# Performance work log

Hardware: AMD Instinct MI355X
Metric: run time of the kernel (lower is better)

## Reference

```python
import jax, jax.numpy as jnp
import numpy as np

NUM_HEADS = 16
HEAD_DIM = 128
CHUNK = 256
ROPE_BASE = 10000.0


def rotate_half(x):
    x1 = x[..., ::2]
    x2 = x[..., 1::2]
    return jnp.stack((-x2, x1), axis=-1).reshape(x.shape)


def rope_cos_sin(seq_len, head_dim):
    inv_freq = 1.0 / (ROPE_BASE ** (np.arange(0, head_dim, 2, dtype=np.float32) / head_dim))
    pos = np.arange(seq_len, dtype=np.float32)
    freqs = np.outer(pos, inv_freq)                  # [S, D/2]
    emb = np.concatenate([freqs, freqs], axis=-1)    # [S, D]
    return jnp.asarray(np.cos(emb)), jnp.asarray(np.sin(emb))


def setup_inputs() -> dict:
    key = jax.random.key(0)
    k1, k2, k3 = jax.random.split(key, 3)
    B, S, E = 2, 4096, 2048
    x = jax.random.normal(k1, (B, S, E), dtype=jnp.float32)
    W_qkv = jax.random.normal(k2, (3 * E, E), dtype=jnp.float32) * 0.02
    W_out = jax.random.normal(k3, (E, E), dtype=jnp.float32) * 0.02
    return {"x": x, "W_qkv": W_qkv, "W_out": W_out}


def reference(x, W_qkv, W_out):
    B, S, E = x.shape
    H, D = NUM_HEADS, HEAD_DIM
    qkv = x @ W_qkv.T                                  # [B,S,3E]
    qkv = qkv.reshape(B, S, 3, H, D).transpose(2, 0, 3, 1, 4)  # [3,B,H,S,D]
    q, k, v = qkv[0], qkv[1], qkv[2]

    cos, sin = rope_cos_sin(S, D)                      # [S,D]
    cos = cos[None, None]
    sin = sin[None, None]
    q = q * cos + rotate_half(q) * sin
    k = k * cos + rotate_half(k) * sin

    # ELU+1 feature map
    q = jax.nn.elu(q) + 1.0
    k = jax.nn.elu(k) + 1.0

    n_chunks = S // CHUNK
    # [n,B,H,C,D]
    to_chunks = lambda t: t.reshape(B, H, n_chunks, CHUNK, D).transpose(2, 0, 1, 3, 4)
    qs, ks, vs = to_chunks(q), to_chunks(k), to_chunks(v)

    tril = jnp.tril(jnp.ones((CHUNK, CHUNK), dtype=x.dtype))  # inclusive causal mask

    def step(carry, qkv_c):
        S_c, Z_c = carry
        qc, kc, vc = qkv_c
        att = jnp.einsum('bhld,bhmd->bhlm', qc, kc) * tril       # intra-chunk causal scores
        num = jnp.einsum('bhlm,bhme->bhle', att, vc) + jnp.einsum('bhld,bhde->bhle', qc, S_c)
        den = att.sum(-1) + jnp.einsum('bhld,bhd->bhl', qc, Z_c)
        S_new = S_c + jnp.einsum('bhld,bhle->bhde', kc, vc)
        Z_new = Z_c + kc.sum(axis=2)
        return (S_new, Z_new), (num, den)

    S0 = jnp.zeros((B, H, D, D), dtype=x.dtype)
    Z0 = jnp.zeros((B, H, D), dtype=x.dtype)
    _, (num, den) = jax.lax.scan(step, (S0, Z0), (qs, ks, vs))
    # num: [n,B,H,C,D] -> [B,H,S,D]; den: [n,B,H,C] -> [B,H,S]
    num = num.transpose(1, 2, 0, 3, 4).reshape(B, H, S, D)
    den = den.transpose(1, 2, 0, 3).reshape(B, H, S)
    den = jnp.maximum(den, 1e-6)

    out = num / den[..., None]                          # [B,H,S,D]
    out = out.transpose(0, 2, 1, 3).reshape(B, S, H * D)
    return out @ W_out.T
```

## Files before the change

kernel.cpp:

```cpp
#include <hip/hip_runtime.h>
#include <cmath>

#define Ss 4096
#define NCh 16
#define CK 256

typedef unsigned short bfu;
typedef __bf16 bf16x8 __attribute__((ext_vector_type(8)));
typedef float f32x4 __attribute__((ext_vector_type(4)));
typedef unsigned short u16x8 __attribute__((ext_vector_type(8)));

__device__ __forceinline__ float bf2f(unsigned short u) {
    union { unsigned u32; float f; } v; v.u32 = ((unsigned)u) << 16; return v.f;
}
__device__ __forceinline__ unsigned short f2bf(float f) {
    union { float f; unsigned u; } v; v.f = f;
    unsigned r = v.u + 0x7fff + ((v.u >> 16) & 1);
    return (unsigned short)(r >> 16);
}

__device__ __forceinline__ void g2l16(void* lds, const void* g) {
    __builtin_amdgcn_global_load_lds(
        (const __attribute__((address_space(1))) void*)g,
        (__attribute__((address_space(3))) void*)lds, 16, 0, 0);
}

#define MFMA __builtin_amdgcn_mfma_f32_16x16x32_bf16

__global__ void rope_table(float* __restrict__ cosT, float* __restrict__ sinT) {
    int id = blockIdx.x * 256 + threadIdx.x;
    int f = id & 63, s = id >> 6;
    float e = (2.0f * (float)f) / 128.0f;
    float inv = 1.0f / powf(10000.0f, e);
    float ang = (float)s * inv;
    cosT[id] = cosf(ang);
    sinT[id] = sinf(ang);
}

__global__ void conv2_bf16(const float* __restrict__ a, bfu* __restrict__ oa, int n4a,
                           const float* __restrict__ b, bfu* __restrict__ ob, int n4b) {
    const int total = n4a + n4b;
    for (int i = blockIdx.x * 256 + threadIdx.x; i < total; i += gridDim.x * 256) {
        const float* in; bfu* out; int j;
        if (i < n4a) { in = a; out = oa; j = i; }
        else         { in = b; out = ob; j = i - n4a; }
        float4 v = ((const float4*)in)[j];
        ushort4 o;
        o.x = f2bf(v.x); o.y = f2bf(v.y); o.z = f2bf(v.z); o.w = f2bf(v.w);
        ((ushort4*)out)[j] = o;
    }
}
__global__ void conv_bf16(const float* __restrict__ in, bfu* __restrict__ out, int n4) {
    for (int i = blockIdx.x * 256 + threadIdx.x; i < n4; i += gridDim.x * 256) {
        float4 v = ((const float4*)in)[i];
        ushort4 o;
        o.x = f2bf(v.x); o.y = f2bf(v.y); o.z = f2bf(v.z); o.w = f2bf(v.w);
        ((ushort4*)out)[i] = o;
    }
}

template<int EPI>
__global__ __launch_bounds__(512) void gemm256(
    const bfu* __restrict__ A, const bfu* __restrict__ B, int nbx,
    const float* __restrict__ cosT, const float* __restrict__ sinT,
    bfu* __restrict__ qb, bfu* __restrict__ kb,
    bfu* __restrict__ kT, bfu* __restrict__ vT,
    float* __restrict__ outF)
{
    __shared__ bfu AsL[2 * 256 * 64];
    __shared__ bfu BsL[2 * 256 * 64];
    const int nwg = gridDim.x;
    const int q8 = nwg >> 3;
    const int swz = (blockIdx.x & 7) * q8 + (blockIdx.x >> 3);
    const int bm = (swz / nbx) * 256, bn = (swz % nbx) * 256;

    const int tid = threadIdx.x;
    const int wid = tid >> 6, lane = tid & 63;
    const int wm = wid >> 2, wn = wid & 3;
    const int l15 = lane & 15, l7 = lane & 7, lhi = lane >> 4;

    const int rl = tid >> 3;
    const int scol = ((tid & 7) ^ (rl & 7)) * 8;
    const bfu* Ab = A + (size_t)(bm + rl) * 2048 + scol;
    const bfu* Bb = B + (size_t)(bn + rl) * 2048 + scol;

    f32x4 acc[8][4] = {};

    auto stageA = [&](int T) {
        bfu* d = AsL + (T & 1) * 16384 + wid * 512;
        const bfu* s = Ab + (size_t)T * 64;
        g2l16(d,         s);
        g2l16(d + 4096,  s + (size_t)64 * 2048);
        g2l16(d + 8192,  s + (size_t)128 * 2048);
        g2l16(d + 12288, s + (size_t)192 * 2048);
    };
    auto stageB = [&](int T) {
        bfu* d = BsL + (T & 1) * 16384 + wid * 512;
        const bfu* s = Bb + (size_t)T * 64;
        g2l16(d,         s);
        g2l16(d + 4096,  s + (size_t)64 * 2048);
        g2l16(d + 8192,  s + (size_t)128 * 2048);
        g2l16(d + 12288, s + (size_t)192 * 2048);
    };

    stageA(0); stageB(0);
    stageA(1); stageB(1);
    asm volatile("s_waitcnt vmcnt(8)" ::: "memory");
    __builtin_amdgcn_s_barrier();
    asm volatile("" ::: "memory");

    for (int T = 0; T < 32; ++T) {
        const char* Ax = (const char*)AsL + (T & 1) * 32768;
        const char* Bx = (const char*)BsL + (T & 1) * 32768;
        bf16x8 a0[4][2], a1[4][2], b0[2][2], b1[2][2];

#pragma unroll
        for (int mi = 0; mi < 4; ++mi)
#pragma unroll
            for (int ks = 0; ks < 2; ++ks)
                a0[mi][ks] = *(const bf16x8*)(Ax + (wm * 128 + mi * 16 + l15) * 128 + (((ks * 4 + lhi) ^ l7) << 4));
#pragma unroll
        for (int ni = 0; ni < 2; ++ni)
#pragma unroll
            for (int ks = 0; ks < 2; ++ks)
                b0[ni][ks] = *(const bf16x8*)(Bx + (wn * 64 + ni * 16 + l15) * 128 + (((ks * 4 + lhi) ^ l7) << 4));
        asm volatile("s_waitcnt lgkmcnt(0)" ::: "memory");
        __builtin_amdgcn_sched_barrier(0);
        __builtin_amdgcn_s_setprio(1);
#pragma unroll
        for (int mi = 0; mi < 4; ++mi)
#pragma unroll
            for (int ni = 0; ni < 2; ++ni) {
                acc[mi][ni] = MFMA(a0[mi][0], b0[ni][0], acc[mi][ni], 0, 0, 0);
                acc[mi][ni] = MFMA(a0[mi][1], b0[ni][1], acc[mi][ni], 0, 0, 0);
            }
        __builtin_amdgcn_s_setprio(0);

#pragma unroll
        for (int ni = 0; ni < 2; ++ni)
#pragma unroll
            for (int ks = 0; ks < 2; ++ks)
                b1[ni][ks] = *(const bf16x8*)(Bx + (wn * 64 + (ni + 2) * 16 + l15) * 128 + (((ks * 4 + lhi) ^ l7) << 4));
        asm volatile("s_waitcnt lgkmcnt(0)" ::: "memory");
        __builtin_amdgcn_sched_barrier(0);
        __builtin_amdgcn_s_setprio(1);
#pragma unroll
        for (int mi = 0; mi < 4; ++mi)
#pragma unroll
            for (int ni = 0; ni < 2; ++ni) {
                acc[mi][ni + 2] = MFMA(a0[mi][0], b1[ni][0], acc[mi][ni + 2], 0, 0, 0);
                acc[mi][ni + 2] = MFMA(a0[mi][1], b1[ni][1], acc[mi][ni + 2], 0, 0, 0);
            }
        __builtin_amdgcn_s_setprio(0);
        __builtin_amdgcn_s_barrier();
        asm volatile("" ::: "memory");

#pragma unroll
        for (int mi = 0; mi < 4; ++mi)
#pragma unroll
            for (int ks = 0; ks < 2; ++ks)
                a1[mi][ks] = *(const bf16x8*)(Ax + (wm * 128 + (mi + 4) * 16 + l15) * 128 + (((ks * 4 + lhi) ^ l7) << 4));
        if (T < 30) stageB(T + 2);
        asm volatile("s_waitcnt lgkmcnt(0)" ::: "memory");
        __builtin_amdgcn_sched_barrier(0);
        __builtin_amdgcn_s_setprio(1);
#pragma unroll
        for (int mi = 0; mi < 4; ++mi)
#pragma unroll
            for (int ni = 0; ni < 2; ++ni) {
                acc[mi + 4][ni] = MFMA(a1[mi][0], b0[ni][0], acc[mi + 4][ni], 0, 0, 0);
                acc[mi + 4][ni] = MFMA(a1[mi][1], b0[ni][1], acc[mi + 4][ni], 0, 0, 0);
            }
        __builtin_amdgcn_s_setprio(0);
        __builtin_amdgcn_s_barrier();
        asm volatile("" ::: "memory");

        if (T < 30) stageA(T + 2);
        __builtin_amdgcn_s_setprio(1);
#pragma unroll
        for (int mi = 0; mi < 4; ++mi)
#pragma unroll
            for (int ni = 0; ni < 2; ++ni) {
                acc[mi + 4][ni + 2] = MFMA(a1[mi][0], b1[ni][0], acc[mi + 4][ni + 2], 0, 0, 0);
                acc[mi + 4][ni + 2] = MFMA(a1[mi][1], b1[ni][1], acc[mi + 4][ni + 2], 0, 0, 0);
            }
        __builtin_amdgcn_s_setprio(0);
        if (T < 30) { asm volatile("s_waitcnt vmcnt(8)" ::: "memory"); }
        else        { asm volatile("s_waitcnt vmcnt(0)" ::: "memory"); }
        __builtin_amdgcn_s_barrier();
        asm volatile("" ::: "memory");
    }

    if constexpr (EPI == 0) {
        const int part = bn >> 11;
#pragma unroll
        for (int mi = 0; mi < 8; ++mi) {
            const int m0 = bm + wm * 128 + mi * 16 + (lhi << 2);
            const int bq = m0 >> 12;
            const int sloc = m0 & 4095;
#pragma unroll
            for (int ni = 0; ni < 4; ++ni) {
                const int cp = (bn & 2047) + wn * 64 + ni * 16 + l15;
                const int d = cp & 127;
                const int head = cp >> 7;
                const int f = d & 63;
                float vv[4];
#pragma unroll
                for (int r = 0; r < 4; ++r) {
                    float v = acc[mi][ni][r];
                    float p = __shfl_xor(v, 1);
                    if (part < 2) {
                        const int s = (m0 + r) & 4095;
                        float cc = cosT[s * 64 + f], sn = sinT[s * 64 + f];
                        float o = (d & 1) ? v * cc + p * sn : v * cc - p * sn;
                        v = o > 0.0f ? o + 1.0f : __expf(o);
                    }
                    vv[r] = v;
                }
                if (part == 0) {
#pragma unroll
                    for (int r = 0; r < 4; ++r)
                        qb[(size_t)(m0 + r) * 2048 + cp] = f2bf(vv[r]);
                } else if (part == 1) {
#pragma unroll
                    for (int r = 0; r < 4; ++r)
                        kb[(size_t)(m0 + r) * 2048 + cp] = f2bf(vv[r]);
                    ushort4 t4;
                    t4.x = f2bf(vv[0]); t4.y = f2bf(vv[1]); t4.z = f2bf(vv[2]); t4.w = f2bf(vv[3]);
                    *(ushort4*)(kT + ((size_t)(bq * 16 + head) * 128 + d) * 4096 + sloc) = t4;
                } else {
                    ushort4 t4;
                    t4.x = f2bf(vv[0]); t4.y = f2bf(vv[1]); t4.z = f2bf(vv[2]); t4.w = f2bf(vv[3]);
                    *(ushort4*)(vT + ((size_t)(bq * 16 + head) * 128 + d) * 4096 + sloc) = t4;
                }
            }
        }
    } else {
#pragma unroll
        for (int mi = 0; mi < 8; ++mi) {
            const int m0 = bm + wm * 128 + mi * 16 + (lhi << 2);
#pragma unroll
            for (int ni = 0; ni < 4; ++ni) {
                const int n = bn + wn * 64 + ni * 16 + l15;
#pragma unroll
                for (int r = 0; r < 4; ++r)
                    outF[(size_t)(m0 + r) * 2048 + n] = acc[mi][ni][r];
            }
        }
    }
}

__global__ __launch_bounds__(256) void kv_outer_mfma(
    const bfu* __restrict__ vT, const bfu* __restrict__ kT,
    bfu* __restrict__ Scb, float* __restrict__ Zc)
{
    __shared__ bfu As[128 * 64];
    __shared__ bfu Bs[128 * 64];
    __shared__ float zS[128][2];
    const int batch = blockIdx.x;
    const int c = batch & 15, h = (batch >> 4) & 15, b = batch >> 8;
    const size_t fbase = (size_t)(b * 16 + h) * 128 * 4096 + c * 256;
    const int tid = threadIdx.x, wid = tid >> 6, lane = tid & 63;
    const int wr = wid >> 1, wc = wid & 1;
    const int srow = lane >> 3, scol = (lane & 7) * 8;
    f32x4 acc[4][4] = {};
    float zreg = 0.0f;
    const int zd = tid >> 1, zo = (tid & 1) * 32;

    for (int k0 = 0; k0 < 256; k0 += 64) {
        __syncthreads();
#pragma unroll
        for (int i = 0; i < 4; ++i) {
            const int r = i * 32 + wid * 8;
            g2l16(&As[r * 64], vT + fbase + (size_t)(r + srow) * 4096 + k0 + scol);
            g2l16(&Bs[r * 64], kT + fbase + (size_t)(r + srow) * 4096 + k0 + scol);
        }
        __syncthreads();
#pragma unroll
        for (int ks = 0; ks < 2; ++ks) {
            bf16x8 af[4], bfr[4];
#pragma unroll
            for (int mi = 0; mi < 4; ++mi)
                af[mi] = *(const bf16x8*)&As[(wr * 64 + mi * 16 + (lane & 15)) * 64 + ks * 32 + (lane >> 4) * 8];
#pragma unroll
            for (int ni = 0; ni < 4; ++ni)
                bfr[ni] = *(const bf16x8*)&Bs[(wc * 64 + ni * 16 + (lane & 15)) * 64 + ks * 32 + (lane >> 4) * 8];
#pragma unroll
            for (int mi = 0; mi < 4; ++mi)
#pragma unroll
                for (int ni = 0; ni < 4; ++ni)
                    acc[mi][ni] = MFMA(af[mi], bfr[ni], acc[mi][ni], 0, 0, 0);
        }
#pragma unroll
        for (int j = 0; j < 32; ++j) zreg += bf2f(Bs[zd * 64 + zo + j]);
    }
    zS[zd][tid & 1] = zreg;
    __syncthreads();
    if (tid < 128) Zc[(size_t)batch * 128 + tid] = zS[tid][0] + zS[tid][1];
    bfu* Sout = Scb + (size_t)batch * 16384;
#pragma unroll
    for (int mi = 0; mi < 4; ++mi)
#pragma unroll
        for (int ni = 0; ni < 4; ++ni) {
            const int d = wc * 64 + ni * 16 + (lane & 15);
#pragma unroll
            for (int r = 0; r < 4; ++r) {
                const int e = wr * 64 + mi * 16 + ((lane >> 4) << 2) + r;
                Sout[e * 128 + d] = f2bf(acc[mi][ni][r]);
            }
        }
}

__global__ void prefix_Sb(bfu* __restrict__ Scb) {
    size_t idx = (size_t)blockIdx.x * 256 + threadIdx.x;
    size_t bh = idx >> 14, de = idx & 16383;
    bfu* p = Scb + bh * (size_t)NCh * 16384 + de;
    float run = 0.0f;
#pragma unroll
    for (int c = 0; c < NCh; ++c) {
        float t = bf2f(p[(size_t)c * 16384]);
        p[(size_t)c * 16384] = f2bf(run);
        run += t;
    }
}
__global__ void prefix_Z(float* __restrict__ Zc) {
    size_t idx = (size_t)blockIdx.x * 256 + threadIdx.x;
    size_t bh = idx >> 7, d = idx & 127;
    float* p = Zc + bh * (size_t)NCh * 128 + d;
    float run = 0.0f;
#pragma unroll
    for (int c = 0; c < NCh; ++c) {
        float t = p[(size_t)c * 128];
        p[(size_t)c * 128] = run;
        run += t;
    }
}

__global__ __launch_bounds__(256) void chunk_mfma(
    const bfu* __restrict__ qb, const bfu* __restrict__ kb,
    const bfu* __restrict__ vT, const bfu* __restrict__ Scb,
    const float* __restrict__ Zc, bfu* __restrict__ ao)
{
    __shared__ bfu shrd[16384];
    __shared__ bfu attL[16384];
    __shared__ float Zs[128];
    __shared__ float denS[128][2];
    const int half = blockIdx.x, batch = blockIdx.y;
    const int c = batch & 15, h = (batch >> 4) & 15, b = batch >> 8;
    const int row0 = b * Ss + c * CK;
    const int tid = threadIdx.x, wid = tid >> 6, lane = tid & 63;
    const int wr = wid >> 1, wc = wid & 1;
    const int sr = lane >> 4, sc8 = (lane & 15) * 8;
    if (tid < 128) Zs[tid] = Zc[(size_t)batch * 128 + tid];

    bf16x8 qf[4][4];
    {
        const bfu* qrow = qb + (size_t)(row0 + half * 128 + wr * 64 + (lane & 15)) * 2048
                          + h * 128 + (lane >> 4) * 8;
#pragma unroll
        for (int mi = 0; mi < 4; ++mi)
#pragma unroll
            for (int ks = 0; ks < 4; ++ks)
                qf[mi][ks] = *(const bf16x8*)(qrow + (size_t)mi * 16 * 2048 + ks * 32);
    }
    f32x4 num[4][4] = {};
    float den_reg = 0.0f;
    const int dl = tid >> 1, dc0 = (tid & 1) * 64;

    for (int kb_ = 0; kb_ <= half; ++kb_) {
        __syncthreads();
#pragma unroll
        for (int i = 0; i < 8; ++i) {
            const int r = i * 16 + wid * 4;
            g2l16(&shrd[r * 128], kb + (size_t)(row0 + kb_ * 128 + r + sr) * 2048 + h * 128 + sc8);
        }
        __syncthreads();
        f32x4 attacc[4][4] = {};
#pragma unroll
        for (int ks = 0; ks < 4; ++ks) {
            bf16x8 bfr[4];
#pragma unroll
            for (int ni = 0; ni < 4; ++ni)
                bfr[ni] = *(const bf16x8*)&shrd[(wc * 64 + ni * 16 + (lane & 15)) * 128 + ks * 32 + (lane >> 4) * 8];
#pragma unroll
            for (int mi = 0; mi < 4; ++mi)
#pragma unroll
                for (int ni = 0; ni < 4; ++ni)
                    attacc[mi][ni] = MFMA(qf[mi][ks], bfr[ni], attacc[mi][ni], 0, 0, 0);
        }
        __syncthreads();
#pragma unroll
        for (int i = 0; i < 8; ++i) {
            const int r = i * 16 + wid * 4;
            g2l16(&shrd[r * 128],
                  vT + ((size_t)(b * 16 + h) * 128 + r + sr) * 4096 + c * 256 + kb_ * 128 + sc8);
        }
        const bool needmask = (kb_ == half);
#pragma unroll
        for (int mi = 0; mi < 4; ++mi)
#pragma unroll
            for (int ni = 0; ni < 4; ++ni) {
                const int l0 = wr * 64 + mi * 16 + ((lane >> 4) << 2);
                const int m = wc * 64 + ni * 16 + (lane & 15);
#pragma unroll
                for (int r = 0; r < 4; ++r) {
                    const int l = l0 + r;
                    float v = attacc[mi][ni][r];
                    if (needmask && (half * 128 + l) < (kb_ * 128 + m)) v = 0.0f;
                    const int byte = (l * 256 + m * 2) ^ ((l & 7) << 4);
                    *(bfu*)((char*)attL + byte) = f2bf(v);
                }
            }
        __syncthreads();
#pragma unroll
        for (int ks = 0; ks < 4; ++ks) {
            bf16x8 af[4], bfr[4];
#pragma unroll
            for (int mi = 0; mi < 4; ++mi) {
                const int l = wr * 64 + mi * 16 + (lane & 15);
                const int byte = (l * 256 + (ks * 32 + (lane >> 4) * 8) * 2) ^ ((l & 7) << 4);
                af[mi] = *(const bf16x8*)((const char*)attL + byte);
            }
#pragma unroll
            for (int ni = 0; ni < 4; ++ni)
                bfr[ni] = *(const bf16x8*)&shrd[(wc * 64 + ni * 16 + (lane & 15)) * 128 + ks * 32 + (lane >> 4) * 8];
#pragma unroll
            for (int mi = 0; mi < 4; ++mi)
#pragma unroll
                for (int ni = 0; ni < 4; ++ni)
                    num[mi][ni] = MFMA(af[mi], bfr[ni], num[mi][ni], 0, 0, 0);
        }
#pragma unroll
        for (int j8 = 0; j8 < 8; ++j8) {
            const int byte = (dl * 256 + (dc0 + j8 * 8) * 2) ^ ((dl & 7) << 4);
            u16x8 a = *(const u16x8*)((const char*)attL + byte);
#pragma unroll
            for (int jj = 0; jj < 8; ++jj) den_reg += bf2f(a[jj]);
        }
    }
    __syncthreads();
#pragma unroll
    for (int i = 0; i < 8; ++i) {
        const int r = i * 16 + wid * 4;
        g2l16(&shrd[r * 128], Scb + (size_t)batch * 16384 + (size_t)(r + sr) * 128 + sc8);
    }
    __syncthreads();
#pragma unroll
    for (int ks = 0; ks < 4; ++ks) {
        bf16x8 bfr[4];
#pragma unroll
        for (int ni = 0; ni < 4; ++ni)
            bfr[ni] = *(const bf16x8*)&shrd[(wc * 64 + ni * 16 + (lane & 15)) * 128 + ks * 32 + (lane >> 4) * 8];
#pragma unroll
        for (int mi = 0; mi < 4; ++mi)
#pragma unroll
            for (int ni = 0; ni < 4; ++ni)
                num[mi][ni] = MFMA(qf[mi][ks], bfr[ni], num[mi][ni], 0, 0, 0);
    }
    {
        const bfu* qrow = qb + (size_t)(row0 + half * 128 + dl) * 2048 + h * 128 + dc0;
#pragma unroll
        for (int j8 = 0; j8 < 8; ++j8) {
            u16x8 a = *(const u16x8*)(qrow + j8 * 8);
#pragma unroll
            for (int jj = 0; jj < 8; ++jj) den_reg += bf2f(a[jj]) * Zs[dc0 + j8 * 8 + jj];
        }
    }
    denS[dl][tid & 1] = den_reg;
    __syncthreads();
    bfu* aop = ao + (size_t)(row0 + half * 128) * 2048 + h * 128;
#pragma unroll
    for (int mi = 0; mi < 4; ++mi)
#pragma unroll
        for (int ni = 0; ni < 4; ++ni) {
            const int e = wc * 64 + ni * 16 + (lane & 15);
#pragma unroll
            for (int r = 0; r < 4; ++r) {
                const int l = wr * 64 + mi * 16 + ((lane >> 4) << 2) + r;
                float dv = denS[l][0] + denS[l][1];
                dv = dv > 1e-6f ? dv : 1e-6f;
                aop[(size_t)l * 2048 + e] = f2bf(num[mi][ni][r] / dv);
            }
        }
}

extern "C" void kernel_launch(void* const* d_in, const int* in_sizes, int n_in,
                              void* d_out, int out_size, void* d_ws, size_t ws_size,
                              hipStream_t stream)
{
    const float* x    = (const float*)d_in[0];
    const float* Wqkv = (const float*)d_in[1];
    const float* Wout = (const float*)d_in[2];
    float* out = (float*)d_out;
    char* ws = (char*)d_ws;

    bfu* xb   = (bfu*)(ws);
    bfu* ao   = (bfu*)(ws);
    bfu* wqb  = (bfu*)(ws + 33554432);
    bfu* wob  = (bfu*)(ws + 33554432);
    float* cosT = (float*)(ws + 58720256);
    float* sinT = (float*)(ws + 59768832);
    bfu* Scb  = (bfu*)(ws + 60817408);
    float* Zc = (float*)(ws + 77594624);
    bfu* qb   = (bfu*)(ws + 77856768);
    bfu* kb   = (bfu*)(ws + 111411200);
    bfu* kTb  = (bfu*)(ws + 144965632);
    bfu* vTb  = (bfu*)(ws + 178520064);

    rope_table<<<1024, 256, 0, stream>>>(cosT, sinT);
    conv2_bf16<<<2048, 256, 0, stream>>>(x, xb, 4194304, Wqkv, wqb, 3145728);
    gemm256<0><<<768, 512, 0, stream>>>(xb, wqb, 24, cosT, sinT, qb, kb, kTb, vTb, nullptr);
    conv_bf16<<<1024, 256, 0, stream>>>(Wout, wob, 1048576);
    kv_outer_mfma<<<512, 256, 0, stream>>>(vTb, kTb, Scb, Zc);
    prefix_Z<<<16, 256, 0, stream>>>(Zc);
    prefix_Sb<<<2048, 256, 0, stream>>>(Scb);
    chunk_mfma<<<dim3(2, 512), 256, 0, stream>>>(qb, kb, vTb, Scb, Zc, ao);
    gemm256<1><<<256, 512, 0, stream>>>(ao, wob, 8, nullptr, nullptr, nullptr, nullptr, nullptr, nullptr, out);
}
```

Baseline: 469.6 us.

## Load GEMM A operand directly from global into registers, bypassing LDS

The A tile is no longer staged through LDS. Each wave now loads its 128-row A slice straight from global memory into registers, prefetching one K-step ahead in two halves interleaved with the MFMA blocks. B stays in a double-buffered LDS stage, with prefetch distance cut from two steps to one and fewer barriers per iteration. This removes the A-side LDS writes and reads and halves shared-memory use. In exchange, the four waves that share a row block each fetch the same A rows, multiplying global/L2 traffic, and global load latency is less hidden.

```diff
diff --git a/kernel.cpp b/kernel.cpp
--- a/kernel.cpp
+++ b/kernel.cpp
@@ -67,7 +67,6 @@
     bfu* __restrict__ kT, bfu* __restrict__ vT,
     float* __restrict__ outF)
 {
-    __shared__ bfu AsL[2 * 256 * 64];
     __shared__ bfu BsL[2 * 256 * 64];
     const int nwg = gridDim.x;
     const int q8 = nwg >> 3;
@@ -81,19 +80,14 @@
 
     const int rl = tid >> 3;
     const int scol = ((tid & 7) ^ (rl & 7)) * 8;
-    const bfu* Ab = A + (size_t)(bm + rl) * 2048 + scol;
     const bfu* Bb = B + (size_t)(bn + rl) * 2048 + scol;
 
+    const bfu* Aw = A + (size_t)(bm + wm * 128 + l15) * 2048 + lhi * 8;
+
     f32x4 acc[8][4] = {};
-
-    auto stageA = [&](int T) {
-        bfu* d = AsL + (T & 1) * 16384 + wid * 512;
-        const bfu* s = Ab + (size_t)T * 64;
-        g2l16(d,         s);
-        g2l16(d + 4096,  s + (size_t)64 * 2048);
-        g2l16(d + 8192,  s + (size_t)128 * 2048);
-        g2l16(d + 12288, s + (size_t)192 * 2048);
-    };
+    bf16x8 a[8][2];
+    bf16x8 b0[2][2], b1[2][2];
+
     auto stageB = [&](int T) {
         bfu* d = BsL + (T & 1) * 16384 + wid * 512;
         const bfu* s = Bb + (size_t)T * 64;
@@ -102,23 +96,26 @@
         g2l16(d + 8192,  s + (size_t)128 * 2048);
         g2l16(d + 12288, s + (size_t)192 * 2048);
     };
-
-    stageA(0); stageB(0);
-    stageA(1); stageB(1);
-    asm volatile("s_waitcnt vmcnt(8)" ::: "memory");
+    auto loadA = [&](int T, int h) {
+#pragma unroll
+        for (int mi = 0; mi < 4; ++mi)
+#pragma unroll
+            for (int ks = 0; ks < 2; ++ks)
+                a[h * 4 + mi][ks] = *(const bf16x8*)(Aw + (size_t)(h * 4 + mi) * 16 * 2048
+                                                     + (size_t)T * 64 + ks * 32);
+    };
+
+    stageB(0);
+    __builtin_amdgcn_sched_barrier(0);
+    loadA(0, 0); loadA(0, 1);
+    __builtin_amdgcn_sched_barrier(0);
+    asm volatile("s_waitcnt vmcnt(16)" ::: "memory");
     __builtin_amdgcn_s_barrier();
     asm volatile("" ::: "memory");
 
     for (int T = 0; T < 32; ++T) {
-        const char* Ax = (const char*)AsL + (T & 1) * 32768;
         const char* Bx = (const char*)BsL + (T & 1) * 32768;
-        bf16x8 a0[4][2], a1[4][2], b0[2][2], b1[2][2];
-
-#pragma unroll
-        for (int mi = 0; mi < 4; ++mi)
-#pragma unroll
-            for (int ks = 0; ks < 2; ++ks)
-                a0[mi][ks] = *(const bf16x8*)(Ax + (wm * 128 + mi * 16 + l15) * 128 + (((ks * 4 + lhi) ^ l7) << 4));
+
 #pragma unroll
         for (int ni = 0; ni < 2; ++ni)
 #pragma unroll
@@ -131,8 +128,8 @@
         for (int mi = 0; mi < 4; ++mi)
 #pragma unroll
             for (int ni = 0; ni < 2; ++ni) {
-                acc[mi][ni] = MFMA(a0[mi][0], b0[ni][0], acc[mi][ni], 0, 0, 0);
-                acc[mi][ni] = MFMA(a0[mi][1], b0[ni][1], acc[mi][ni], 0, 0, 0);
+                acc[mi][ni] = MFMA(a[mi][0], b0[ni][0], acc[mi][ni], 0, 0, 0);
+                acc[mi][ni] = MFMA(a[mi][1], b0[ni][1], acc[mi][ni], 0, 0, 0);
             }
         __builtin_amdgcn_s_setprio(0);
 
@@ -148,45 +145,41 @@
         for (int mi = 0; mi < 4; ++mi)
 #pragma unroll
             for (int ni = 0; ni < 2; ++ni) {
-                acc[mi][ni + 2] = MFMA(a0[mi][0], b1[ni][0], acc[mi][ni + 2], 0, 0, 0);
-                acc[mi][ni + 2] = MFMA(a0[mi][1], b1[ni][1], acc[mi][ni + 2], 0, 0, 0);
+                acc[mi][ni + 2] = MFMA(a[mi][0], b1[ni][0], acc[mi][ni + 2], 0, 0, 0);
+                acc[mi][ni + 2] = MFMA(a[mi][1], b1[ni][1], acc[mi][ni + 2], 0, 0, 0);
             }
         __builtin_amdgcn_s_setprio(0);
-        __builtin_amdgcn_s_barrier();
-        asm volatile("" ::: "memory");
-
-#pragma unroll
-        for (int mi = 0; mi < 4; ++mi)
-#pragma unroll
-            for (int ks = 0; ks < 2; ++ks)
-                a1[mi][ks] = *(const bf16x8*)(Ax + (wm * 128 + (mi + 4) * 16 + l15) * 128 + (((ks * 4 + lhi) ^ l7) << 4));
-        if (T < 30) stageB(T + 2);
-        asm volatile("s_waitcnt lgkmcnt(0)" ::: "memory");
-        __builtin_amdgcn_sched_barrier(0);
+
+        if (T < 31) {
+            stageB(T + 1);
+            __builtin_amdgcn_sched_barrier(0);
+            loadA(T + 1, 0);
+            __builtin_amdgcn_sched_barrier(0);
+        }
         __builtin_amdgcn_s_setprio(1);
 #pragma unroll
         for (int mi = 0; mi < 4; ++mi)
 #pragma unroll
             for (int ni = 0; ni < 2; ++ni) {
-                acc[mi + 4][ni] = MFMA(a1[mi][0], b0[ni][0], acc[mi + 4][ni], 0, 0, 0);
-                acc[mi + 4][ni] = MFMA(a1[mi][1], b0[ni][1], acc[mi + 4][ni], 0, 0, 0);
+                acc[mi + 4][ni] = MFMA(a[mi + 4][0], b0[ni][0], acc[mi + 4][ni], 0, 0, 0);
+                acc[mi + 4][ni] = MFMA(a[mi + 4][1], b0[ni][1], acc[mi + 4][ni], 0, 0, 0);
             }
         __builtin_amdgcn_s_setprio(0);
-        __builtin_amdgcn_s_barrier();
-        asm volatile("" ::: "memory");
-
-        if (T < 30) stageA(T + 2);
+
         __builtin_amdgcn_s_setprio(1);
 #pragma unroll
         for (int mi = 0; mi < 4; ++mi)
 #pragma unroll
             for (int ni = 0; ni < 2; ++ni) {
-                acc[mi + 4][ni + 2] = MFMA(a1[mi][0], b1[ni][0], acc[mi + 4][ni + 2], 0, 0, 0);
-                acc[mi + 4][ni + 2] = MFMA(a1[mi][1], b1[ni][1], acc[mi + 4][ni + 2], 0, 0, 0);
+                acc[mi + 4][ni + 2] = MFMA(a[mi + 4][0], b1[ni][0], acc[mi + 4][ni + 2], 0, 0, 0);
+                acc[mi + 4][ni + 2] = MFMA(a[mi + 4][1], b1[ni][1], acc[mi + 4][ni + 2], 0, 0, 0);
             }
         __builtin_amdgcn_s_setprio(0);
-        if (T < 30) { asm volatile("s_waitcnt vmcnt(8)" ::: "memory"); }
-        else        { asm volatile("s_waitcnt vmcnt(0)" ::: "memory"); }
+        if (T < 31) {
+            loadA(T + 1, 1);
+            __builtin_amdgcn_sched_barrier(0);
+            asm volatile("s_waitcnt vmcnt(8)" ::: "memory");
+        }
         __builtin_amdgcn_s_barrier();
         asm volatile("" ::: "memory");
     }
```

New measurement: 723.5 us. 1.54x slower.

## Use 4-wave GEMM with 128x128 per-wave tiles and pipelined A fragment loads

Applied to the files above, without the earlier changes.

The 256x256 GEMM block drops from 8 waves to 4, so each wave computes a 128x128 output tile with 64 accumulators. All B fragments are held in registers and A fragments are double-buffered in groups, with partial lgkmcnt waits to overlap LDS reads with MFMA. Both A and B tiles are now staged once per K step after a barrier, rather than interleaved between MFMA phases. This raises register-level data reuse and cuts LDS read traffic per MFMA. The cost is heavy VGPR/AGPR pressure, one block per CU, and less overlap of global loads with compute.

```diff
diff --git a/kernel.cpp b/kernel.cpp
--- a/kernel.cpp
+++ b/kernel.cpp
@@ -60,7 +60,7 @@
 }
 
 template<int EPI>
-__global__ __launch_bounds__(512) void gemm256(
+__global__ __launch_bounds__(256, 1) void gemm256(
     const bfu* __restrict__ A, const bfu* __restrict__ B, int nbx,
     const float* __restrict__ cosT, const float* __restrict__ sinT,
     bfu* __restrict__ qb, bfu* __restrict__ kb,
@@ -76,7 +76,7 @@
 
     const int tid = threadIdx.x;
     const int wid = tid >> 6, lane = tid & 63;
-    const int wm = wid >> 2, wn = wid & 3;
+    const int wm = wid >> 1, wn = wid & 1;
     const int l15 = lane & 15, l7 = lane & 7, lhi = lane >> 4;
 
     const int rl = tid >> 3;
@@ -84,109 +84,77 @@
     const bfu* Ab = A + (size_t)(bm + rl) * 2048 + scol;
     const bfu* Bb = B + (size_t)(bn + rl) * 2048 + scol;
 
-    f32x4 acc[8][4] = {};
+    f32x4 acc[8][8] = {};
+    bf16x8 bfr[8][2];
+    bf16x8 av[2][2][2];
 
     auto stageA = [&](int T) {
         bfu* d = AsL + (T & 1) * 16384 + wid * 512;
         const bfu* s = Ab + (size_t)T * 64;
-        g2l16(d,         s);
-        g2l16(d + 4096,  s + (size_t)64 * 2048);
-        g2l16(d + 8192,  s + (size_t)128 * 2048);
-        g2l16(d + 12288, s + (size_t)192 * 2048);
+#pragma unroll
+        for (int i = 0; i < 8; ++i)
+            g2l16(d + i * 2048, s + (size_t)i * 32 * 2048);
     };
     auto stageB = [&](int T) {
         bfu* d = BsL + (T & 1) * 16384 + wid * 512;
         const bfu* s = Bb + (size_t)T * 64;
-        g2l16(d,         s);
-        g2l16(d + 4096,  s + (size_t)64 * 2048);
-        g2l16(d + 8192,  s + (size_t)128 * 2048);
-        g2l16(d + 12288, s + (size_t)192 * 2048);
+#pragma unroll
+        for (int i = 0; i < 8; ++i)
+            g2l16(d + i * 2048, s + (size_t)i * 32 * 2048);
     };
 
     stageA(0); stageB(0);
     stageA(1); stageB(1);
-    asm volatile("s_waitcnt vmcnt(8)" ::: "memory");
+    asm volatile("s_waitcnt vmcnt(16)" ::: "memory");
     __builtin_amdgcn_s_barrier();
     asm volatile("" ::: "memory");
 
     for (int T = 0; T < 32; ++T) {
         const char* Ax = (const char*)AsL + (T & 1) * 32768;
         const char* Bx = (const char*)BsL + (T & 1) * 32768;
-        bf16x8 a0[4][2], a1[4][2], b0[2][2], b1[2][2];
-
-#pragma unroll
-        for (int mi = 0; mi < 4; ++mi)
+
+#pragma unroll
+        for (int ni = 0; ni < 8; ++ni)
 #pragma unroll
             for (int ks = 0; ks < 2; ++ks)
-                a0[mi][ks] = *(const bf16x8*)(Ax + (wm * 128 + mi * 16 + l15) * 128 + (((ks * 4 + lhi) ^ l7) << 4));
-#pragma unroll
-        for (int ni = 0; ni < 2; ++ni)
+                bfr[ni][ks] = *(const bf16x8*)(Bx + (wn * 128 + ni * 16 + l15) * 128 + (((ks * 4 + lhi) ^ l7) << 4));
+#pragma unroll
+        for (int mi2 = 0; mi2 < 2; ++mi2)
 #pragma unroll
             for (int ks = 0; ks < 2; ++ks)
-                b0[ni][ks] = *(const bf16x8*)(Bx + (wn * 64 + ni * 16 + l15) * 128 + (((ks * 4 + lhi) ^ l7) << 4));
-        asm volatile("s_waitcnt lgkmcnt(0)" ::: "memory");
-        __builtin_amdgcn_sched_barrier(0);
-        __builtin_amdgcn_s_setprio(1);
-#pragma unroll
-        for (int mi = 0; mi < 4; ++mi)
-#pragma unroll
-            for (int ni = 0; ni < 2; ++ni) {
-                acc[mi][ni] = MFMA(a0[mi][0], b0[ni][0], acc[mi][ni], 0, 0, 0);
-                acc[mi][ni] = MFMA(a0[mi][1], b0[ni][1], acc[mi][ni], 0, 0, 0);
-            }
-        __builtin_amdgcn_s_setprio(0);
-
-#pragma unroll
-        for (int ni = 0; ni < 2; ++ni)
-#pragma unroll
-            for (int ks = 0; ks < 2; ++ks)
-                b1[ni][ks] = *(const bf16x8*)(Bx + (wn * 64 + (ni + 2) * 16 + l15) * 128 + (((ks * 4 + lhi) ^ l7) << 4));
-        asm volatile("s_waitcnt lgkmcnt(0)" ::: "memory");
-        __builtin_amdgcn_sched_barrier(0);
-        __builtin_amdgcn_s_setprio(1);
-#pragma unroll
-        for (int mi = 0; mi < 4; ++mi)
-#pragma unroll
-            for (int ni = 0; ni < 2; ++ni) {
-                acc[mi][ni + 2] = MFMA(a0[mi][0], b1[ni][0], acc[mi][ni + 2], 0, 0, 0);
-                acc[mi][ni + 2] = MFMA(a0[mi][1], b1[ni][1], acc[mi][ni + 2], 0, 0, 0);
-            }
-        __builtin_amdgcn_s_setprio(0);
+                av[0][mi2][ks] = *(const bf16x8*)(Ax + (wm * 128 + mi2 * 16 + l15) * 128 + (((ks * 4 + lhi) ^ l7) << 4));
+
+#pragma unroll
+        for (int g = 0; g < 4; ++g) {
+            if (g < 3) {
+#pragma unroll
+                for (int mi2 = 0; mi2 < 2; ++mi2)
+#pragma unroll
+                    for (int ks = 0; ks < 2; ++ks)
+                        av[(g + 1) & 1][mi2][ks] = *(const bf16x8*)(Ax + (wm * 128 + ((g + 1) * 2 + mi2) * 16 + l15) * 128 + (((ks * 4 + lhi) ^ l7) << 4));
+                asm volatile("s_waitcnt lgkmcnt(4)" ::: "memory");
+            } else {
+                asm volatile("s_waitcnt lgkmcnt(0)" ::: "memory");
+            }
+            __builtin_amdgcn_sched_barrier(0);
+            __builtin_amdgcn_s_setprio(1);
+#pragma unroll
+            for (int mi2 = 0; mi2 < 2; ++mi2)
+#pragma unroll
+                for (int ni = 0; ni < 8; ++ni) {
+                    acc[g * 2 + mi2][ni] = MFMA(av[g & 1][mi2][0], bfr[ni][0], acc[g * 2 + mi2][ni], 0, 0, 0);
+                    acc[g * 2 + mi2][ni] = MFMA(av[g & 1][mi2][1], bfr[ni][1], acc[g * 2 + mi2][ni], 0, 0, 0);
+                }
+            __builtin_amdgcn_s_setprio(0);
+        }
+
         __builtin_amdgcn_s_barrier();
-        asm volatile("" ::: "memory");
-
-#pragma unroll
-        for (int mi = 0; mi < 4; ++mi)
-#pragma unroll
-            for (int ks = 0; ks < 2; ++ks)
-                a1[mi][ks] = *(const bf16x8*)(Ax + (wm * 128 + (mi + 4) * 16 + l15) * 128 + (((ks * 4 + lhi) ^ l7) << 4));
-        if (T < 30) stageB(T + 2);
-        asm volatile("s_waitcnt lgkmcnt(0)" ::: "memory");
-        __builtin_amdgcn_sched_barrier(0);
-        __builtin_amdgcn_s_setprio(1);
-#pragma unroll
-        for (int mi = 0; mi < 4; ++mi)
-#pragma unroll
-            for (int ni = 0; ni < 2; ++ni) {
-                acc[mi + 4][ni] = MFMA(a1[mi][0], b0[ni][0], acc[mi + 4][ni], 0, 0, 0);
-                acc[mi + 4][ni] = MFMA(a1[mi][1], b0[ni][1], acc[mi + 4][ni], 0, 0, 0);
-            }
-        __builtin_amdgcn_s_setprio(0);
-        __builtin_amdgcn_s_barrier();
-        asm volatile("" ::: "memory");
-
-        if (T < 30) stageA(T + 2);
-        __builtin_amdgcn_s_setprio(1);
-#pragma unroll
-        for (int mi = 0; mi < 4; ++mi)
-#pragma unroll
-            for (int ni = 0; ni < 2; ++ni) {
-                acc[mi + 4][ni + 2] = MFMA(a1[mi][0], b1[ni][0], acc[mi + 4][ni + 2], 0, 0, 0);
-                acc[mi + 4][ni + 2] = MFMA(a1[mi][1], b1[ni][1], acc[mi + 4][ni + 2], 0, 0, 0);
-            }
-        __builtin_amdgcn_s_setprio(0);
-        if (T < 30) { asm volatile("s_waitcnt vmcnt(8)" ::: "memory"); }
-        else        { asm volatile("s_waitcnt vmcnt(0)" ::: "memory"); }
+        if (T < 30) {
+            stageA(T + 2); stageB(T + 2);
+            asm volatile("s_waitcnt vmcnt(16)" ::: "memory");
+        } else if (T == 30) {
+            asm volatile("s_waitcnt vmcnt(0)" ::: "memory");
+        }
         __builtin_amdgcn_s_barrier();
         asm volatile("" ::: "memory");
     }
@@ -199,8 +167,8 @@
             const int bq = m0 >> 12;
             const int sloc = m0 & 4095;
 #pragma unroll
-            for (int ni = 0; ni < 4; ++ni) {
-                const int cp = (bn & 2047) + wn * 64 + ni * 16 + l15;
+            for (int ni = 0; ni < 8; ++ni) {
+                const int cp = (bn & 2047) + wn * 128 + ni * 16 + l15;
                 const int d = cp & 127;
                 const int head = cp >> 7;
                 const int f = d & 63;
@@ -240,8 +208,8 @@
         for (int mi = 0; mi < 8; ++mi) {
             const int m0 = bm + wm * 128 + mi * 16 + (lhi << 2);
 #pragma unroll
-            for (int ni = 0; ni < 4; ++ni) {
-                const int n = bn + wn * 64 + ni * 16 + l15;
+            for (int ni = 0; ni < 8; ++ni) {
+                const int n = bn + wn * 128 + ni * 16 + l15;
 #pragma unroll
                 for (int r = 0; r < 4; ++r)
                     outF[(size_t)(m0 + r) * 2048 + n] = acc[mi][ni][r];
@@ -509,11 +477,11 @@
 
     rope_table<<<1024, 256, 0, stream>>>(cosT, sinT);
     conv2_bf16<<<2048, 256, 0, stream>>>(x, xb, 4194304, Wqkv, wqb, 3145728);
-    gemm256<0><<<768, 512, 0, stream>>>(xb, wqb, 24, cosT, sinT, qb, kb, kTb, vTb, nullptr);
+    gemm256<0><<<768, 256, 0, stream>>>(xb, wqb, 24, cosT, sinT, qb, kb, kTb, vTb, nullptr);
     conv_bf16<<<1024, 256, 0, stream>>>(Wout, wob, 1048576);
     kv_outer_mfma<<<512, 256, 0, stream>>>(vTb, kTb, Scb, Zc);
     prefix_Z<<<16, 256, 0, stream>>>(Zc);
     prefix_Sb<<<2048, 256, 0, stream>>>(Scb);
     chunk_mfma<<<dim3(2, 512), 256, 0, stream>>>(qb, kb, vTb, Scb, Zc, ao);
-    gemm256<1><<<256, 512, 0, stream>>>(ao, wob, 8, nullptr, nullptr, nullptr, nullptr, nullptr, nullptr, out);
-}
+    gemm256<1><<<256, 256, 0, stream>>>(ao, wob, 8, nullptr, nullptr, nullptr, nullptr, nullptr, nullptr, out);
+}
```

Result: slower. 682.4 us (+45.3%).
